# Kernel tuning notes

Hardware: AMD Instinct MI355X
Metric: run time of the kernel (lower is better)

Reference implementation:

```python
import jax, jax.numpy as jnp
import numpy as np

B, C, H, W = 8, 256, 64, 64
EPS = 1e-5


def _mk_conv_bn(key, oc, ic):
    k = jax.random.split(key, 6)
    return dict(
        w=jax.random.normal(k[0], (oc, ic), jnp.float32) * 0.01,  # trunc-normal approx, stddev 0.01
        b=jnp.zeros((oc,), jnp.float32),
        s=jax.random.uniform(k[1], (oc,), jnp.float32, 0.5, 1.5),   # BN scale
        t=jax.random.normal(k[2], (oc,), jnp.float32) * 0.1,        # BN shift
        m=jax.random.normal(k[3], (oc,), jnp.float32) * 0.1,        # BN running mean
        v=jax.random.uniform(k[4], (oc,), jnp.float32, 0.5, 1.5),   # BN running var
    )


def setup_inputs() -> dict:
    key = jax.random.key(0)
    ks = jax.random.split(key, 6)
    d = {"x": jax.random.normal(ks[0], (B, C, H, W), jnp.float32)}
    for i, (oc, ic) in zip([1, 2, 3, 4], [(C // 8, C), (C // 8, C), (C // 2, C), (C, C // 2)]):
        p = _mk_conv_bn(ks[i], oc, ic)
        for name, val in p.items():
            d[f"{name}{i}"] = val
    d["gamma"] = jnp.asarray(0.5, jnp.float32)
    return d


def _cbn(x, w, b, s, t, m, v, relu=True):
    # conv1x1 + BatchNorm(eval) [+ ReLU]; dropout is identity at inference
    y = jnp.einsum('bchw,oc->bohw', x, w) + b[None, :, None, None]
    scale = (s / jnp.sqrt(v + EPS))[None, :, None, None]
    y = (y - m[None, :, None, None]) * scale + t[None, :, None, None]
    return jax.nn.relu(y) if relu else y


def _maxpool2(x):
    b, c, h, w = x.shape
    return x.reshape(b, c, h // 2, 2, w // 2, 2).max(axis=(3, 5))


def reference(x, w1, b1, s1, t1, m1, v1, w2, b2, s2, t2, m2, v2,
              w3, b3, s3, t3, m3, v3, w4, b4, s4, t4, m4, v4, gamma):
    b, c, h, w = x.shape
    f = _maxpool2(_cbn(x, w1, b1, s1, t1, m1, v1))   # (B, C/8, H/2, W/2)
    g = _cbn(x, w2, b2, s2, t2, m2, v2)              # (B, C/8, H, W)
    hh = _maxpool2(_cbn(x, w3, b3, s3, t3, m3, v3))  # (B, C/2, H/2, W/2)
    hw, hw4 = h * w, (h // 2) * (w // 2)
    f = f.reshape(b, c // 8, hw4).transpose(0, 2, 1)  # (B, HW/4, C/8)
    g = g.reshape(b, c // 8, hw)                      # (B, C/8, HW)
    s = jnp.einsum('bnk,bkm->bnm', f, g)              # (B, HW/4, HW)
    beta = jax.nn.softmax(s, axis=1)                  # softmax over dim=1, as in source
    hh = hh.reshape(b, c // 2, hw4)                   # (B, C/2, HW/4)
    o = jnp.einsum('bcn,bnm->bcm', hh, beta).reshape(b, c // 2, h, w)
    out = _cbn(o, w4, b4, s4, t4, m4, v4, relu=False)
    return gamma * out + x
```

## Files before the change

kernel.cpp:

```cpp
#include <hip/hip_runtime.h>
#include <hip/hip_bf16.h>

#define HW   4096
#define HW4  1024
#define EPS  1e-5f
#define SM_SHIFT 20.0f

typedef __attribute__((ext_vector_type(8))) short bf16x8;
typedef __attribute__((ext_vector_type(4))) float f32x4;

__device__ __forceinline__ short f2bs(float f) {
    union { float f; unsigned u; } v; v.f = f;
    unsigned r = v.u + 0x7FFFu + ((v.u >> 16) & 1u);
    return (short)(r >> 16);
}
__device__ __forceinline__ int swz64(int r, int c)  { return (r << 6) + ((c ^ (r & 7))  << 3); }
__device__ __forceinline__ int swz128(int r, int c) { return (r << 7) + ((c ^ (r & 15)) << 3); }
__device__ __forceinline__ int p40(int r, int c)    { return r * 40 + c * 8; }

__global__ __launch_bounds__(256) void conv123pool(
    const float* __restrict__ x,
    const float* __restrict__ w1, const float* __restrict__ b1, const float* __restrict__ s1,
    const float* __restrict__ t1, const float* __restrict__ m1, const float* __restrict__ v1,
    const float* __restrict__ w2, const float* __restrict__ b2, const float* __restrict__ s2,
    const float* __restrict__ t2, const float* __restrict__ m2, const float* __restrict__ v2,
    const float* __restrict__ w3, const float* __restrict__ b3, const float* __restrict__ s3,
    const float* __restrict__ t3, const float* __restrict__ m3, const float* __restrict__ v3,
    short* __restrict__ gbuf, short* __restrict__ fbuf, short* __restrict__ hhbuf)
{
    __shared__ __align__(16) short Wl[96 * 64];
    __shared__ __align__(16) short Xl[128 * 64];
    __shared__ float alB[96], beB[96];

    const int t = threadIdx.x;
    const int lane = t & 63, wv = t >> 6;
    const int quad = lane >> 4, l16 = lane & 15;
    const int ptile = blockIdx.x;
    const int ocg   = blockIdx.y;
    const int bz    = blockIdx.z;
    const int pBase = ptile * 128;
    const int wcol  = (wv & 1) * 32;
    const int woch  = (wv >> 1) * 48;

    if (t < 96) {
        int j = ocg * 96 + t;
        float pb, ps, ptv, pm, pv;
        if (j < 32)      { pb = b1[j]; ps = s1[j]; ptv = t1[j]; pm = m1[j]; pv = v1[j]; }
        else if (j < 64) { int c = j - 32; pb = b2[c]; ps = s2[c]; ptv = t2[c]; pm = m2[c]; pv = v2[c]; }
        else             { int c = j - 64; pb = b3[c]; ps = s3[c]; ptv = t3[c]; pm = m3[c]; pv = v3[c]; }
        float al = ps * rsqrtf(pv + EPS);
        alB[t] = al; beB[t] = (pb - pm) * al + ptv;
    }

    const f32x4 fzero = {0.f, 0.f, 0.f, 0.f};
    f32x4 acc[3][4];
    #pragma unroll
    for (int i = 0; i < 3; ++i)
        #pragma unroll
        for (int j = 0; j < 4; ++j) acc[i][j] = fzero;

    const int ptOff0 = wcol, ptOff1 = wcol + 16, ptOff2 = wcol + 64, ptOff3 = wcol + 80;
    const int xp  = t & 127, xk8 = t >> 7;

    for (int k0 = 0; k0 < 256; k0 += 64) {
        #pragma unroll
        for (int i = 0; i < 2; ++i) {
            int idx = t + i * 256;
            if (i == 0 || t < 128) {
                int oc = idx >> 2, kb = (idx & 3) * 16;
                int j = ocg * 96 + oc;
                const float* wp = (j < 32) ? (w1 + j * 256)
                                : (j < 64) ? (w2 + (j - 32) * 256)
                                           : (w3 + (j - 64) * 256);
                wp += k0 + kb;
                float4 a = *(const float4*)(wp);
                float4 b = *(const float4*)(wp + 4);
                float4 c = *(const float4*)(wp + 8);
                float4 d = *(const float4*)(wp + 12);
                bf16x8 lo, hi;
                lo[0]=f2bs(a.x); lo[1]=f2bs(a.y); lo[2]=f2bs(a.z); lo[3]=f2bs(a.w);
                lo[4]=f2bs(b.x); lo[5]=f2bs(b.y); lo[6]=f2bs(b.z); lo[7]=f2bs(b.w);
                hi[0]=f2bs(c.x); hi[1]=f2bs(c.y); hi[2]=f2bs(c.z); hi[3]=f2bs(c.w);
                hi[4]=f2bs(d.x); hi[5]=f2bs(d.y); hi[6]=f2bs(d.z); hi[7]=f2bs(d.w);
                *(bf16x8*)&Wl[swz64(oc, (kb >> 3))]     = lo;
                *(bf16x8*)&Wl[swz64(oc, (kb >> 3) + 1)] = hi;
            }
        }
        {
            const float* xp0 = x + ((size_t)bz * 256 + k0 + xk8 * 32) * HW + pBase + xp;
            float fv[32];
            #pragma unroll
            for (int i = 0; i < 32; ++i) fv[i] = xp0[(size_t)i * HW];
            #pragma unroll
            for (int c = 0; c < 4; ++c) {
                bf16x8 v;
                #pragma unroll
                for (int jj = 0; jj < 8; ++jj) v[jj] = f2bs(fv[c * 8 + jj]);
                *(bf16x8*)&Xl[swz64(xp, xk8 * 4 + c)] = v;
            }
        }
        __syncthreads();
        #pragma unroll
        for (int kk = 0; kk < 2; ++kk) {
            bf16x8 bfr[4];
            bfr[0] = *(const bf16x8*)&Xl[swz64(ptOff0 + l16, kk * 4 + quad)];
            bfr[1] = *(const bf16x8*)&Xl[swz64(ptOff1 + l16, kk * 4 + quad)];
            bfr[2] = *(const bf16x8*)&Xl[swz64(ptOff2 + l16, kk * 4 + quad)];
            bfr[3] = *(const bf16x8*)&Xl[swz64(ptOff3 + l16, kk * 4 + quad)];
            #pragma unroll
            for (int tt = 0; tt < 3; ++tt) {
                bf16x8 afr = *(const bf16x8*)&Wl[swz64(woch + tt * 16 + l16, kk * 4 + quad)];
                #pragma unroll
                for (int pt = 0; pt < 4; ++pt)
                    acc[tt][pt] = __builtin_amdgcn_mfma_f32_16x16x32_bf16(afr, bfr[pt], acc[tt][pt], 0, 0, 0);
            }
        }
        __syncthreads();
    }

    #pragma unroll
    for (int tt = 0; tt < 3; ++tt) {
        #pragma unroll
        for (int r = 0; r < 4; ++r) {
            int ocl = woch + tt * 16 + quad * 4 + r;
            int j = ocg * 96 + ocl;
            float al = alB[ocl], be = beB[ocl];
            float y[4];
            y[0] = fmaxf(acc[tt][0][r] * al + be, 0.f);
            y[1] = fmaxf(acc[tt][1][r] * al + be, 0.f);
            y[2] = fmaxf(acc[tt][2][r] * al + be, 0.f);
            y[3] = fmaxf(acc[tt][3][r] * al + be, 0.f);
            if (j >= 32 && j < 64) {
                size_t base = ((size_t)bz * 32 + (j - 32)) * HW + pBase;
                gbuf[base + ptOff0 + l16] = f2bs(y[0]);
                gbuf[base + ptOff1 + l16] = f2bs(y[1]);
                gbuf[base + ptOff2 + l16] = f2bs(y[2]);
                gbuf[base + ptOff3 + l16] = f2bs(y[3]);
            } else {
                #pragma unroll
                for (int c = 0; c < 2; ++c) {
                    float v  = fmaxf(y[c], y[c + 2]);
                    float po = fmaxf(v, __shfl_xor(v, 1));
                    if ((l16 & 1) == 0) {
                        int col = wcol + c * 16 + l16;
                        int n = ptile * 32 + (col >> 1);
                        if (j < 32) fbuf[((size_t)bz * 32 + j) * HW4 + n] = f2bs(po);
                        else        hhbuf[((size_t)bz * 128 + (j - 64)) * HW4 + n] = f2bs(po);
                    }
                }
            }
        }
    }
}

__global__ __launch_bounds__(256, 4) void attn_conv4(
    const short* __restrict__ gbuf,
    const short* __restrict__ fbuf,
    const short* __restrict__ hhbuf,
    const float* __restrict__ x,
    const float* __restrict__ w4, const float* __restrict__ b4, const float* __restrict__ s4,
    const float* __restrict__ t4, const float* __restrict__ m4, const float* __restrict__ v4,
    const float* __restrict__ gamma, float* __restrict__ out)
{
    __shared__ __align__(16) short smem[18432];
    __shared__ float alB4[256], beB4[256];
    short* gTl = smem;
    short* fTl = smem + 2560;
    short* sTl = smem + 5120;
    short* hhl = smem + 9216;
    short* o_l = smem;
    short* Wl4 = smem + 8192;

    const int t = threadIdx.x;
    const int lane = t & 63, wv = t >> 6;
    const int quad = lane >> 4, l16 = lane & 15;
    const int bz = blockIdx.y;
    const int m0 = blockIdx.x * 64;
    const int ms = wv * 16;
    const f32x4 fzero = {0.f, 0.f, 0.f, 0.f};

    {
        float al = s4[t] * rsqrtf(v4[t] + EPS);
        alB4[t] = al; beB4[t] = (b4[t] - m4[t]) * al + t4[t];
    }

    {
        int mm = t & 63, k8 = t >> 6;
        bf16x8 v;
        #pragma unroll
        for (int j = 0; j < 8; ++j)
            v[j] = gbuf[((size_t)bz * 32 + k8 * 8 + j) * HW + m0 + mm];
        *(bf16x8*)&gTl[p40(mm, k8)] = v;
    }
    __syncthreads();
    bf16x8 bg = *(const bf16x8*)&gTl[p40(ms + l16, quad)];

    const int fnn = t & 63, fk8 = t >> 6;
    const int hrow = t >> 3, hnc = t & 7;
    const short* fB = fbuf + (size_t)bz * 32 * HW4;
    const short* hB = hhbuf + (size_t)bz * 128 * HW4;

    float psum = 0.f;
    f32x4 oacc[8];
    #pragma unroll
    for (int i = 0; i < 8; ++i) oacc[i] = fzero;

    for (int n0 = 0; n0 < 1024; n0 += 64) {
        __syncthreads();
        {
            bf16x8 v;
            #pragma unroll
            for (int j = 0; j < 8; ++j)
                v[j] = fB[(fk8 * 8 + j) * HW4 + n0 + fnn];
            *(bf16x8*)&fTl[p40(fnn, fk8)] = v;
        }
        {
            #pragma unroll
            for (int i = 0; i < 4; ++i)
                *(bf16x8*)&hhl[swz64(i * 32 + hrow, hnc)] =
                    *(const bf16x8*)(hB + (size_t)(i * 32 + hrow) * HW4 + n0 + hnc * 8);
        }
        __syncthreads();

        f32x4 sacc[4];
        #pragma unroll
        for (int nt = 0; nt < 4; ++nt) {
            bf16x8 af = *(const bf16x8*)&fTl[p40(nt * 16 + l16, quad)];
            sacc[nt] = __builtin_amdgcn_mfma_f32_16x16x32_bf16(af, bg, fzero, 0, 0, 0);
        }

        #pragma unroll
        for (int nt = 0; nt < 4; ++nt) {
            short4 ev;
            #pragma unroll
            for (int r = 0; r < 4; ++r) {
                float e = __expf(sacc[nt][r] - SM_SHIFT);
                psum += e;
                ((short*)&ev)[r] = f2bs(e);
            }
            int chunk = nt * 2 + (quad >> 1);
            *(short4*)&sTl[swz64(ms + l16, chunk) + (quad & 1) * 4] = ev;
        }

        #pragma unroll
        for (int kk = 0; kk < 2; ++kk) {
            bf16x8 bs = *(const bf16x8*)&sTl[swz64(ms + l16, kk * 4 + quad)];
            #pragma unroll
            for (int ct = 0; ct < 8; ++ct) {
                bf16x8 ah = *(const bf16x8*)&hhl[swz64(ct * 16 + l16, kk * 4 + quad)];
                oacc[ct] = __builtin_amdgcn_mfma_f32_16x16x32_bf16(ah, bs, oacc[ct], 0, 0, 0);
            }
        }
    }
    __syncthreads();

    psum += __shfl_xor(psum, 16);
    psum += __shfl_xor(psum, 32);
    {
        float inv = 1.0f / psum;
        int m = ms + l16;
        #pragma unroll
        for (int ct = 0; ct < 8; ++ct) {
            short4 ov;
            #pragma unroll
            for (int r = 0; r < 4; ++r) ((short*)&ov)[r] = f2bs(oacc[ct][r] * inv);
            *(short4*)&o_l[swz128(m, ct * 2 + (quad >> 1)) + (quad & 1) * 4] = ov;
        }
    }

    f32x4 acc4[4][4];
    #pragma unroll
    for (int i = 0; i < 4; ++i)
        #pragma unroll
        for (int j = 0; j < 4; ++j) acc4[i][j] = fzero;

    #pragma unroll
    for (int k0 = 0; k0 < 128; k0 += 32) {
        __syncthreads();
        {
            const float* wp = w4 + t * 128 + k0;
            #pragma unroll
            for (int c = 0; c < 4; ++c) {
                float4 a = *(const float4*)(wp + c * 8);
                float4 b = *(const float4*)(wp + c * 8 + 4);
                bf16x8 v;
                v[0]=f2bs(a.x); v[1]=f2bs(a.y); v[2]=f2bs(a.z); v[3]=f2bs(a.w);
                v[4]=f2bs(b.x); v[5]=f2bs(b.y); v[6]=f2bs(b.z); v[7]=f2bs(b.w);
                *(bf16x8*)&Wl4[p40(t, c)] = v;
            }
        }
        __syncthreads();
        bf16x8 bfr[4];
        #pragma unroll
        for (int mt = 0; mt < 4; ++mt)
            bfr[mt] = *(const bf16x8*)&o_l[swz128(mt * 16 + l16, (k0 >> 3) + quad)];
        #pragma unroll
        for (int ot = 0; ot < 4; ++ot) {
            bf16x8 afr = *(const bf16x8*)&Wl4[p40(wv * 64 + ot * 16 + l16, quad)];
            #pragma unroll
            for (int mt = 0; mt < 4; ++mt)
                acc4[ot][mt] = __builtin_amdgcn_mfma_f32_16x16x32_bf16(afr, bfr[mt], acc4[ot][mt], 0, 0, 0);
        }
    }

    float gm = gamma[0];
    #pragma unroll
    for (int ot = 0; ot < 4; ++ot) {
        #pragma unroll
        for (int r = 0; r < 4; ++r) {
            int oc = wv * 64 + ot * 16 + quad * 4 + r;
            float al = alB4[oc], be = beB4[oc];
            #pragma unroll
            for (int mt = 0; mt < 4; ++mt) {
                int p = m0 + mt * 16 + l16;
                float y  = acc4[ot][mt][r] * al + be;
                float xo = x[((size_t)bz * 256 + oc) * HW + p];
                out[((size_t)bz * 256 + oc) * HW + p] = gm * y + xo;
            }
        }
    }
}

extern "C" void kernel_launch(void* const* d_in, const int* in_sizes, int n_in,
                              void* d_out, int out_size, void* d_ws, size_t ws_size,
                              hipStream_t stream)
{
    const float* x  = (const float*)d_in[0];
    const float* w1 = (const float*)d_in[1];
    const float* b1 = (const float*)d_in[2];
    const float* s1 = (const float*)d_in[3];
    const float* t1 = (const float*)d_in[4];
    const float* m1 = (const float*)d_in[5];
    const float* v1 = (const float*)d_in[6];
    const float* w2 = (const float*)d_in[7];
    const float* b2 = (const float*)d_in[8];
    const float* s2 = (const float*)d_in[9];
    const float* t2 = (const float*)d_in[10];
    const float* m2 = (const float*)d_in[11];
    const float* v2 = (const float*)d_in[12];
    const float* w3 = (const float*)d_in[13];
    const float* b3 = (const float*)d_in[14];
    const float* s3 = (const float*)d_in[15];
    const float* t3 = (const float*)d_in[16];
    const float* m3 = (const float*)d_in[17];
    const float* v3 = (const float*)d_in[18];
    const float* w4 = (const float*)d_in[19];
    const float* b4 = (const float*)d_in[20];
    const float* s4 = (const float*)d_in[21];
    const float* t4 = (const float*)d_in[22];
    const float* m4 = (const float*)d_in[23];
    const float* v4 = (const float*)d_in[24];
    const float* gm = (const float*)d_in[25];
    float* out = (float*)d_out;

    short* gbuf  = (short*)d_ws;
    short* fbuf  = gbuf  + (size_t)8 * 32 * 4096;
    short* hhbuf = fbuf  + (size_t)8 * 32 * 1024;

    conv123pool<<<dim3(32, 2, 8), 256, 0, stream>>>(
        x, w1, b1, s1, t1, m1, v1, w2, b2, s2, t2, m2, v2, w3, b3, s3, t3, m3, v3,
        gbuf, fbuf, hhbuf);
    attn_conv4<<<dim3(64, 8), 256, 0, stream>>>(
        gbuf, fbuf, hhbuf, x, w4, b4, s4, t4, m4, v4, gm, out);
}
```

Before: 171.4 us.

## Prefetch attention operands into registers and double-buffer hh tiles

Stores the pooled f projection transposed, so the attention kernel can load MFMA A-fragments for the scores straight from global memory into registers instead of staging them through LDS. The hh tiles are register-prefetched one iteration ahead and written into alternating LDS buffers, which drops one barrier per loop iteration. The conv4 weights are converted to bf16 once, inside the first kernel, and register-prefetched per k-slice in the second. Occupancy hint drops from 4 to 2 blocks and LDS use grows. The uncoalesced transposed f writes and lower occupancy may offset some of the gain.

```diff
diff --git a/kernel.cpp b/kernel.cpp
--- a/kernel.cpp
+++ b/kernel.cpp
@@ -26,7 +26,9 @@
     const float* __restrict__ t2, const float* __restrict__ m2, const float* __restrict__ v2,
     const float* __restrict__ w3, const float* __restrict__ b3, const float* __restrict__ s3,
     const float* __restrict__ t3, const float* __restrict__ m3, const float* __restrict__ v3,
-    short* __restrict__ gbuf, short* __restrict__ fbuf, short* __restrict__ hhbuf)
+    const float* __restrict__ w4,
+    short* __restrict__ w4T,
+    short* __restrict__ gbuf, short* __restrict__ fbufT, short* __restrict__ hhbuf)
 {
     __shared__ __align__(16) short Wl[96 * 64];
     __shared__ __align__(16) short Xl[128 * 64];
@@ -41,6 +43,14 @@
     const int pBase = ptile * 128;
     const int wcol  = (wv & 1) * 32;
     const int woch  = (wv >> 1) * 48;
+
+    if (ocg == 0 && bz == 0) {
+        int idx = (ptile * 256 + t) * 4;
+        float4 a = *(const float4*)(w4 + idx);
+        short4 o;
+        o.x = f2bs(a.x); o.y = f2bs(a.y); o.z = f2bs(a.z); o.w = f2bs(a.w);
+        *(short4*)&w4T[idx] = o;
+    }
 
     if (t < 96) {
         int j = ocg * 96 + t;
@@ -144,7 +154,7 @@
                     if ((l16 & 1) == 0) {
                         int col = wcol + c * 16 + l16;
                         int n = ptile * 32 + (col >> 1);
-                        if (j < 32) fbuf[((size_t)bz * 32 + j) * HW4 + n] = f2bs(po);
+                        if (j < 32) fbufT[((size_t)bz * 1024 + n) * 32 + j] = f2bs(po);
                         else        hhbuf[((size_t)bz * 128 + (j - 64)) * HW4 + n] = f2bs(po);
                     }
                 }
@@ -153,23 +163,23 @@
     }
 }
 
-__global__ __launch_bounds__(256, 4) void attn_conv4(
+__global__ __launch_bounds__(256, 2) void attn_conv4(
     const short* __restrict__ gbuf,
-    const short* __restrict__ fbuf,
+    const short* __restrict__ fbufT,
     const short* __restrict__ hhbuf,
     const float* __restrict__ x,
-    const float* __restrict__ w4, const float* __restrict__ b4, const float* __restrict__ s4,
+    const short* __restrict__ w4T, const float* __restrict__ b4, const float* __restrict__ s4,
     const float* __restrict__ t4, const float* __restrict__ m4, const float* __restrict__ v4,
     const float* __restrict__ gamma, float* __restrict__ out)
 {
-    __shared__ __align__(16) short smem[18432];
+    __shared__ __align__(16) short smem[23040];
     __shared__ float alB4[256], beB4[256];
-    short* gTl = smem;
-    short* fTl = smem + 2560;
-    short* sTl = smem + 5120;
-    short* hhl = smem + 9216;
-    short* o_l = smem;
-    short* Wl4 = smem + 8192;
+    short* gTl  = smem;
+    short* sTl  = smem + 2560;
+    short* hhl0 = smem + 6656;
+    short* hhl1 = smem + 14848;
+    short* o_l  = smem;
+    short* Wl4  = smem + 8192;
 
     const int t = threadIdx.x;
     const int lane = t & 63, wv = t >> 6;
@@ -184,6 +194,18 @@
         alB4[t] = al; beB4[t] = (b4[t] - m4[t]) * al + t4[t];
     }
 
+    const short* fT = fbufT + (size_t)bz * 1024 * 32;
+    const short* hB = hhbuf + (size_t)bz * 128 * HW4;
+    const int hrow = t >> 3, hnc = t & 7;
+
+    bf16x8 fr[4], hr[4];
+    #pragma unroll
+    for (int nt = 0; nt < 4; ++nt)
+        fr[nt] = *(const bf16x8*)&fT[(nt * 16 + l16) * 32 + quad * 8];
+    #pragma unroll
+    for (int i = 0; i < 4; ++i)
+        hr[i] = *(const bf16x8*)(hB + (size_t)(i * 32 + hrow) * HW4 + hnc * 8);
+
     {
         int mm = t & 63, k8 = t >> 6;
         bf16x8 v;
@@ -195,39 +217,31 @@
     __syncthreads();
     bf16x8 bg = *(const bf16x8*)&gTl[p40(ms + l16, quad)];
 
-    const int fnn = t & 63, fk8 = t >> 6;
-    const int hrow = t >> 3, hnc = t & 7;
-    const short* fB = fbuf + (size_t)bz * 32 * HW4;
-    const short* hB = hhbuf + (size_t)bz * 128 * HW4;
-
     float psum = 0.f;
     f32x4 oacc[8];
     #pragma unroll
     for (int i = 0; i < 8; ++i) oacc[i] = fzero;
 
-    for (int n0 = 0; n0 < 1024; n0 += 64) {
-        __syncthreads();
-        {
-            bf16x8 v;
-            #pragma unroll
-            for (int j = 0; j < 8; ++j)
-                v[j] = fB[(fk8 * 8 + j) * HW4 + n0 + fnn];
-            *(bf16x8*)&fTl[p40(fnn, fk8)] = v;
-        }
-        {
-            #pragma unroll
-            for (int i = 0; i < 4; ++i)
-                *(bf16x8*)&hhl[swz64(i * 32 + hrow, hnc)] =
-                    *(const bf16x8*)(hB + (size_t)(i * 32 + hrow) * HW4 + n0 + hnc * 8);
-        }
+    #pragma unroll 2
+    for (int it = 0; it < 16; ++it) {
+        const int n0n = ((it + 1) & 15) << 6;
+        short* hb = (it & 1) ? hhl1 : hhl0;
+
+        #pragma unroll
+        for (int i = 0; i < 4; ++i)
+            *(bf16x8*)&hb[swz64(i * 32 + hrow, hnc)] = hr[i];
+        #pragma unroll
+        for (int i = 0; i < 4; ++i)
+            hr[i] = *(const bf16x8*)(hB + (size_t)(i * 32 + hrow) * HW4 + n0n + hnc * 8);
         __syncthreads();
 
         f32x4 sacc[4];
         #pragma unroll
-        for (int nt = 0; nt < 4; ++nt) {
-            bf16x8 af = *(const bf16x8*)&fTl[p40(nt * 16 + l16, quad)];
-            sacc[nt] = __builtin_amdgcn_mfma_f32_16x16x32_bf16(af, bg, fzero, 0, 0, 0);
-        }
+        for (int nt = 0; nt < 4; ++nt)
+            sacc[nt] = __builtin_amdgcn_mfma_f32_16x16x32_bf16(fr[nt], bg, fzero, 0, 0, 0);
+        #pragma unroll
+        for (int nt = 0; nt < 4; ++nt)
+            fr[nt] = *(const bf16x8*)&fT[(n0n + nt * 16 + l16) * 32 + quad * 8];
 
         #pragma unroll
         for (int nt = 0; nt < 4; ++nt) {
@@ -247,7 +261,7 @@
             bf16x8 bs = *(const bf16x8*)&sTl[swz64(ms + l16, kk * 4 + quad)];
             #pragma unroll
             for (int ct = 0; ct < 8; ++ct) {
-                bf16x8 ah = *(const bf16x8*)&hhl[swz64(ct * 16 + l16, kk * 4 + quad)];
+                bf16x8 ah = *(const bf16x8*)&hb[swz64(ct * 16 + l16, kk * 4 + quad)];
                 oacc[ct] = __builtin_amdgcn_mfma_f32_16x16x32_bf16(ah, bs, oacc[ct], 0, 0, 0);
             }
         }
@@ -274,20 +288,23 @@
         #pragma unroll
         for (int j = 0; j < 4; ++j) acc4[i][j] = fzero;
 
-    #pragma unroll
-    for (int k0 = 0; k0 < 128; k0 += 32) {
-        __syncthreads();
-        {
-            const float* wp = w4 + t * 128 + k0;
-            #pragma unroll
-            for (int c = 0; c < 4; ++c) {
-                float4 a = *(const float4*)(wp + c * 8);
-                float4 b = *(const float4*)(wp + c * 8 + 4);
-                bf16x8 v;
-                v[0]=f2bs(a.x); v[1]=f2bs(a.y); v[2]=f2bs(a.z); v[3]=f2bs(a.w);
-                v[4]=f2bs(b.x); v[5]=f2bs(b.y); v[6]=f2bs(b.z); v[7]=f2bs(b.w);
-                *(bf16x8*)&Wl4[p40(t, c)] = v;
-            }
+    const int wrow = t >> 2, wcid = t & 3;
+    bf16x8 Wr[4];
+    #pragma unroll
+    for (int g = 0; g < 4; ++g)
+        Wr[g] = *(const bf16x8*)(w4T + (g * 64 + wrow) * 128 + wcid * 8);
+
+    #pragma unroll
+    for (int k0i = 0; k0i < 4; ++k0i) {
+        const int k0 = k0i * 32;
+        __syncthreads();
+        #pragma unroll
+        for (int g = 0; g < 4; ++g)
+            *(bf16x8*)&Wl4[p40(g * 64 + wrow, wcid)] = Wr[g];
+        if (k0i < 3) {
+            #pragma unroll
+            for (int g = 0; g < 4; ++g)
+                Wr[g] = *(const bf16x8*)(w4T + (g * 64 + wrow) * 128 + k0 + 32 + wcid * 8);
         }
         __syncthreads();
         bf16x8 bfr[4];
@@ -354,12 +371,13 @@
     float* out = (float*)d_out;
 
     short* gbuf  = (short*)d_ws;
-    short* fbuf  = gbuf  + (size_t)8 * 32 * 4096;
-    short* hhbuf = fbuf  + (size_t)8 * 32 * 1024;
+    short* fbufT = gbuf  + (size_t)8 * 32 * 4096;
+    short* hhbuf = fbufT + (size_t)8 * 1024 * 32;
+    short* w4T   = hhbuf + (size_t)8 * 128 * 1024;
 
     conv123pool<<<dim3(32, 2, 8), 256, 0, stream>>>(
         x, w1, b1, s1, t1, m1, v1, w2, b2, s2, t2, m2, v2, w3, b3, s3, t3, m3, v3,
-        gbuf, fbuf, hhbuf);
+        w4, w4T, gbuf, fbufT, hhbuf);
     attn_conv4<<<dim3(64, 8), 256, 0, stream>>>(
-        gbuf, fbuf, hhbuf, x, w4, b4, s4, t4, m4, v4, gm, out);
+        gbuf, fbufT, hhbuf, x, w4T, b4, s4, t4, m4, v4, gm, out);
 }
```

Result: faster. 164.4 us (-4.1%).
